# Kernel optimization log

Measured on AMD Instinct MI355X. Metric: run time of the kernel, lower is better.

The kernel has to match this reference:

```python
import jax, jax.numpy as jnp
import numpy as np

N = 100000
E = 3200000
IN_C, HID_C, LAT_C = 256, 256, 64
NEG_SLOPE = 0.01  # torch nn.LeakyReLU default


def gcn_conv(x, W, b, src, dst, norm):
    # x: [N, Fin], W: [Fin, Fout], src/dst: [E'] (self-loops included), norm: [E']
    h = x @ W                                   # [N, Fout]
    msg = h[src] * norm[:, None]                # gather + scale
    out = jax.ops.segment_sum(msg, dst, num_segments=N)  # scatter-add
    return out + b


def _with_self_loops(edge_index):
    loop = jnp.arange(N, dtype=edge_index.dtype)
    src = jnp.concatenate([edge_index[0], loop])
    dst = jnp.concatenate([edge_index[1], loop])
    return src, dst


def _sym_norm(src, dst):
    ones = jnp.ones(src.shape[0], dtype=jnp.float32)
    deg = jax.ops.segment_sum(ones, dst, num_segments=N)  # in-degree incl. self-loop
    dis = jnp.where(deg > 0, jax.lax.rsqrt(deg), 0.0)
    return dis[src] * dis[dst]


def setup_inputs() -> dict:
    key = jax.random.key(0)
    ks = jax.random.split(key, 8)
    x = jax.random.normal(ks[0], (N, IN_C), dtype=jnp.float32)
    edge_index = jax.random.randint(ks[1], (2, E), 0, N, dtype=jnp.int64)
    s = 1.0 / np.sqrt(IN_C)
    W_shared = jax.random.uniform(ks[2], (IN_C, HID_C), jnp.float32, -s, s)
    b_shared = jnp.zeros((HID_C,), jnp.float32)
    s2 = 1.0 / np.sqrt(HID_C)
    W_mu = jax.random.uniform(ks[3], (HID_C, LAT_C), jnp.float32, -s2, s2)
    b_mu = jnp.zeros((LAT_C,), jnp.float32)
    W_lv = jax.random.uniform(ks[4], (HID_C, LAT_C), jnp.float32, -s2, s2)
    b_lv = jnp.zeros((LAT_C,), jnp.float32)
    return {"x": x, "edge_index": edge_index,
            "W_shared": W_shared, "b_shared": b_shared,
            "W_mu": W_mu, "b_mu": b_mu,
            "W_lv": W_lv, "b_lv": b_lv}


def reference(x, W_shared, b_shared, W_mu, b_mu, W_lv, b_lv, edge_index):
    src, dst = _with_self_loops(edge_index)
    norm = _sym_norm(src, dst)
    h = gcn_conv(x, W_shared, b_shared, src, dst, norm)
    h = jnp.where(h >= 0, h, NEG_SLOPE * h)     # LeakyReLU(0.01)
    mu = gcn_conv(h, W_mu, b_mu, src, dst, norm)
    logvar = jnp.minimum(gcn_conv(h, W_lv, b_lv, src, dst, norm), 10.0)
    return (mu, logvar)
```

## Files before the change

kernel.cpp:

```cpp
#include <hip/hip_runtime.h>
#include <hip/hip_bf16.h>

#define N_NODES 100000
#define FEAT 256
#define NEG_SLOPE 0.01f
#define NBUK 782
#define BCAP 5120

using bf16x8 = __attribute__((ext_vector_type(8))) __bf16;
using f32x4  = __attribute__((ext_vector_type(4))) float;
using ushort8 = __attribute__((ext_vector_type(8))) unsigned short;

__device__ __forceinline__ unsigned short f2bf(float f) {
    unsigned int u = __float_as_uint(f);
    unsigned int r = u + 0x7fffu + ((u >> 16) & 1u);
    return (unsigned short)(r >> 16);
}
__device__ __forceinline__ void gload_lds16(const void* g, void* l) {
    __builtin_amdgcn_global_load_lds(
        (const __attribute__((address_space(1))) void*)g,
        (__attribute__((address_space(3))) void*)l, 16, 0, 0);
}
__device__ __forceinline__ void accum_row(float* acc, uint4 u, float qv) {
    unsigned int dw[4] = {u.x, u.y, u.z, u.w};
#pragma unroll
    for (int d = 0; d < 4; ++d) {
        acc[d * 4 + 0] += qv * (float)(dw[d] & 0xffu);
        acc[d * 4 + 1] += qv * (float)((dw[d] >> 8) & 0xffu);
        acc[d * 4 + 2] += qv * (float)((dw[d] >> 16) & 0xffu);
        acc[d * 4 + 3] += qv * (float)(dw[d] >> 24);
    }
}

__global__ void k_detect(const int* __restrict__ ei, int* __restrict__ flag) {
    if (threadIdx.x == 0) {
        int nz = 0;
        for (int i = 0; i < 64; ++i) nz |= ei[2 * i + 1];
        *flag = (nz == 0) ? 2 : 1;
    }
}

__global__ void k_bucket(const int* __restrict__ ei, const int* __restrict__ flag,
                         int* __restrict__ bcnt, int2* __restrict__ ebuf, int E) {
    __shared__ int lcnt[NBUK];
    __shared__ int lbase[NBUK];
    const int t = threadIdx.x;
    const int s = *flag;
    for (int i = t; i < NBUK; i += 256) lcnt[i] = 0;
    __syncthreads();
    const int per = (E + gridDim.x - 1) / gridDim.x;
    const int e0 = blockIdx.x * per;
    const int e1 = min(e0 + per, E);
    for (int e = e0 + t; e < e1; e += 256) {
        const int d = ei[(size_t)(E + e) * s];
        atomicAdd(&lcnt[d >> 7], 1);
    }
    __syncthreads();
    for (int i = t; i < NBUK; i += 256) {
        const int c = lcnt[i];
        lbase[i] = c ? atomicAdd(&bcnt[i], c) : 0;
        lcnt[i] = 0;
    }
    __syncthreads();
    for (int e = e0 + t; e < e1; e += 256) {
        const int sv = ei[(size_t)e * s];
        const int dv = ei[(size_t)(E + e) * s];
        const int b = dv >> 7;
        const int p = lbase[b] + atomicAdd(&lcnt[b], 1);
        if (p < BCAP) ebuf[(size_t)b * BCAP + p] = make_int2(sv, dv);
    }
}

__global__ void k_csr(const int2* __restrict__ ebuf, const int* __restrict__ bcnt,
                      int* __restrict__ csr, int* __restrict__ rowp0,
                      int* __restrict__ rowe, float* __restrict__ dis) {
    __shared__ int ncnt[128];
    __shared__ int nexcl[128];
    __shared__ int nstart[128];
    const int t = threadIdx.x;
    const int b = blockIdx.x;
    const int nb = b << 7;
    if (t < 128) ncnt[t] = 0;
    __syncthreads();
    const int cnt = min(bcnt[b], BCAP);
    const int2* eb = ebuf + (size_t)b * BCAP;
    for (int i = t; i < cnt; i += 256) atomicAdd(&ncnt[eb[i].y - nb], 1);
    __syncthreads();
    const int own = (t < 128) ? ncnt[t] : 0;
    const int region = (t < 128) ? ((own + 4) & ~3) : 0;
    if (t < 128) nexcl[t] = region;
    __syncthreads();
    for (int off = 1; off < 128; off <<= 1) {
        int v = 0;
        if (t < 128 && t >= off) v = nexcl[t - off];
        __syncthreads();
        if (t < 128) nexcl[t] += v;
        __syncthreads();
    }
    if (t < 128) {
        const int excl = nexcl[t] - region;
        const int v = nb + t;
        if (v < N_NODES) {
            rowp0[v] = b * BCAP + excl;
            rowe[v]  = b * BCAP + excl + region;
            dis[v]   = rsqrtf((float)(own + 1));
            if (excl < BCAP) csr[(size_t)b * BCAP + excl] = v;
            for (int i = own + 1; i < region; ++i)
                if (excl + i < BCAP) csr[(size_t)b * BCAP + excl + i] = N_NODES;
        }
        nstart[t] = excl + 1;
        ncnt[t] = 0;
    }
    __syncthreads();
    for (int i = t; i < cnt; i += 256) {
        const int2 e = eb[i];
        const int li = e.y - nb;
        const int p = nstart[li] + atomicAdd(&ncnt[li], 1);
        if (p < BCAP) csr[(size_t)b * BCAP + p] = e.x;
    }
}

__global__ void k_cvt_w(const float* __restrict__ Wsh, const float* __restrict__ Wmu,
                        const float* __restrict__ Wlv,
                        unsigned short* __restrict__ Wt, unsigned short* __restrict__ Wct) {
    const int i = blockIdx.x * 256 + threadIdx.x;
    {
        const int n = i >> 8, k = i & 255;
        Wt[(size_t)n * 256 + k] = f2bf(Wsh[(size_t)k * 256 + n]);
    }
    if (i < 128 * 256) {
        const int n = i >> 8, k = i & 255;
        const float v = (n < 64) ? Wmu[(size_t)k * 64 + n] : Wlv[(size_t)k * 64 + (n - 64)];
        Wct[(size_t)n * 256 + k] = f2bf(v);
    }
}

__global__ void __launch_bounds__(512) k_gemm256f(
        const float* __restrict__ A, const unsigned short* __restrict__ Bt,
        unsigned char* __restrict__ q8, float* __restrict__ qs,
        const float* __restrict__ scale, int M) {
    __shared__ __align__(16) unsigned short lA[128 * 32];
    __shared__ __align__(16) unsigned short lB[256 * 32];
    __shared__ float rmax[128][4];
    const int t = threadIdx.x;
    const int w = t >> 6, l = t & 63;
    const int wr = w >> 2, wc = w & 3;
    const int l15 = l & 15, lh = l >> 4;
    const int rowbase = blockIdx.x * 128;

    f32x4 acc[4][4];
#pragma unroll
    for (int mi = 0; mi < 4; ++mi)
#pragma unroll
        for (int nj = 0; nj < 4; ++nj)
            acc[mi][nj] = (f32x4){0.f, 0.f, 0.f, 0.f};

    const int ar = t >> 2, sl = t & 3;
    int grA = rowbase + ar; if (grA > M - 1) grA = M - 1;
    const float* aptr = A + (size_t)grA * FEAT + sl * 8;

#pragma unroll 1
    for (int ks = 0; ks < 8; ++ks) {
        const int k0 = ks * 32;
        gload_lds16(Bt + ((size_t)ar * FEAT + k0 + sl * 8), &lB[(size_t)t * 8]);
        gload_lds16(Bt + ((size_t)(128 + ar) * FEAT + k0 + sl * 8), &lB[(size_t)(512 + t) * 8]);
        float4 f0 = *reinterpret_cast<const float4*>(aptr + k0);
        float4 f1 = *reinterpret_cast<const float4*>(aptr + k0 + 4);
        ushort8 ua;
        ua[0] = f2bf(f0.x); ua[1] = f2bf(f0.y); ua[2] = f2bf(f0.z); ua[3] = f2bf(f0.w);
        ua[4] = f2bf(f1.x); ua[5] = f2bf(f1.y); ua[6] = f2bf(f1.z); ua[7] = f2bf(f1.w);
        *reinterpret_cast<ushort8*>(&lA[(size_t)ar * 32 + sl * 8]) = ua;
        asm volatile("s_waitcnt vmcnt(0)" ::: "memory");
        __syncthreads();

        bf16x8 a[4];
#pragma unroll
        for (int mi = 0; mi < 4; ++mi)
            a[mi] = *reinterpret_cast<const bf16x8*>(&lA[(wr * 64 + mi * 16 + l15) * 32 + lh * 8]);
#pragma unroll
        for (int nj = 0; nj < 4; ++nj) {
            bf16x8 b = *reinterpret_cast<const bf16x8*>(&lB[(wc * 64 + nj * 16 + l15) * 32 + lh * 8]);
#pragma unroll
            for (int mi = 0; mi < 4; ++mi)
                acc[mi][nj] = __builtin_amdgcn_mfma_f32_16x16x32_bf16(a[mi], b, acc[mi][nj], 0, 0, 0);
        }
        __syncthreads();
    }

#pragma unroll
    for (int mi = 0; mi < 4; ++mi) {
#pragma unroll
        for (int r = 0; r < 4; ++r) {
            const int rl = wr * 64 + mi * 16 + lh * 4 + r;
            int row = rowbase + rl; if (row > M - 1) row = M - 1;
            const float sc = scale[row];
            float m = 0.f;
#pragma unroll
            for (int nj = 0; nj < 4; ++nj) {
                acc[mi][nj][r] *= sc;
                m = fmaxf(m, fabsf(acc[mi][nj][r]));
            }
            m = fmaxf(m, __shfl_xor(m, 1, 64));
            m = fmaxf(m, __shfl_xor(m, 2, 64));
            m = fmaxf(m, __shfl_xor(m, 4, 64));
            m = fmaxf(m, __shfl_xor(m, 8, 64));
            if (l15 == 0) rmax[rl][wc] = m;
        }
    }
    __syncthreads();
#pragma unroll
    for (int mi = 0; mi < 4; ++mi) {
#pragma unroll
        for (int r = 0; r < 4; ++r) {
            const int rl = wr * 64 + mi * 16 + lh * 4 + r;
            const int row = rowbase + rl;
            const float fm = fmaxf(fmaxf(rmax[rl][0], rmax[rl][1]),
                                   fmaxf(rmax[rl][2], rmax[rl][3]));
            const float inv = (fm > 0.f) ? (127.0f / fm) : 0.f;
            if (row < M) {
                if (wc == 0 && l15 == 0) qs[row] = fm * (1.0f / 127.0f);
#pragma unroll
                for (int nj = 0; nj < 4; ++nj) {
                    int qv = (int)rintf(acc[mi][nj][r] * inv) + 128;
                    qv = min(max(qv, 0), 255);
                    q8[(size_t)row * 256 + wc * 64 + nj * 16 + l15] = (unsigned char)qv;
                }
            }
        }
    }
}

__global__ void k_gemm128q(const unsigned short* __restrict__ A,
                           const unsigned short* __restrict__ Bt,
                           unsigned char* __restrict__ q8, float* __restrict__ qs,
                           const float* __restrict__ scale, int M) {
    __shared__ __align__(16) unsigned short lA[64 * 32];
    __shared__ __align__(16) unsigned short lB[128 * 32];
    __shared__ float rmax[64][4];
    const int t = threadIdx.x;
    const int w = t >> 6, l = t & 63;
    const int l15 = l & 15, lh = l >> 4;
    const int rowbase = blockIdx.x * 64;

    f32x4 acc[4][2];
#pragma unroll
    for (int mi = 0; mi < 4; ++mi)
#pragma unroll
        for (int nj = 0; nj < 2; ++nj)
            acc[mi][nj] = (f32x4){0.f, 0.f, 0.f, 0.f};

    const int sr = t >> 2, sl = t & 3;
    int grA = rowbase + sr; if (grA > M - 1) grA = M - 1;

#pragma unroll 1
    for (int ks = 0; ks < 8; ++ks) {
        const int k0 = ks * 32;
        gload_lds16(A + ((size_t)grA * FEAT + k0 + sl * 8), &lA[(size_t)t * 8]);
#pragma unroll
        for (int j = 0; j < 2; ++j)
            gload_lds16(Bt + ((size_t)(j * 64 + sr) * FEAT + k0 + sl * 8),
                        &lB[(size_t)j * 2048 + (size_t)t * 8]);
        asm volatile("s_waitcnt vmcnt(0)" ::: "memory");
        __syncthreads();

        bf16x8 a[4];
#pragma unroll
        for (int mi = 0; mi < 4; ++mi)
            a[mi] = *reinterpret_cast<const bf16x8*>(&lA[(mi * 16 + l15) * 32 + lh * 8]);
#pragma unroll
        for (int nj = 0; nj < 2; ++nj) {
            bf16x8 b = *reinterpret_cast<const bf16x8*>(&lB[(w * 32 + nj * 16 + l15) * 32 + lh * 8]);
#pragma unroll
            for (int mi = 0; mi < 4; ++mi)
                acc[mi][nj] = __builtin_amdgcn_mfma_f32_16x16x32_bf16(a[mi], b, acc[mi][nj], 0, 0, 0);
        }
        __syncthreads();
    }

#pragma unroll
    for (int mi = 0; mi < 4; ++mi) {
#pragma unroll
        for (int r = 0; r < 4; ++r) {
            const int rl = mi * 16 + lh * 4 + r;
            int row = rowbase + rl; if (row > M - 1) row = M - 1;
            const float sc = scale[row];
            float m = 0.f;
#pragma unroll
            for (int nj = 0; nj < 2; ++nj) {
                acc[mi][nj][r] *= sc;
                m = fmaxf(m, fabsf(acc[mi][nj][r]));
            }
            m = fmaxf(m, __shfl_xor(m, 1, 64));
            m = fmaxf(m, __shfl_xor(m, 2, 64));
            m = fmaxf(m, __shfl_xor(m, 4, 64));
            m = fmaxf(m, __shfl_xor(m, 8, 64));
            if (l15 == 0) rmax[rl][w] = m;
        }
    }
    __syncthreads();
#pragma unroll
    for (int mi = 0; mi < 4; ++mi) {
#pragma unroll
        for (int r = 0; r < 4; ++r) {
            const int rl = mi * 16 + lh * 4 + r;
            const int row = rowbase + rl;
            const float fm = fmaxf(fmaxf(rmax[rl][0], rmax[rl][1]),
                                   fmaxf(rmax[rl][2], rmax[rl][3]));
            const float inv = (fm > 0.f) ? (127.0f / fm) : 0.f;
            if (row < M) {
                if (w == 0 && l15 == 0) qs[row] = fm * (1.0f / 127.0f);
#pragma unroll
                for (int nj = 0; nj < 2; ++nj) {
                    int qv = (int)rintf(acc[mi][nj][r] * inv) + 128;
                    qv = min(max(qv, 0), 255);
                    q8[(size_t)row * 128 + w * 32 + nj * 16 + l15] = (unsigned char)qv;
                }
            }
        }
    }
}

__global__ void k_agg1(const unsigned char* __restrict__ q8, const float* __restrict__ qs,
                       const int* __restrict__ rowp0, const int* __restrict__ rowe,
                       const int* __restrict__ csr,
                       const float* __restrict__ dis, const float* __restrict__ bias,
                       unsigned short* __restrict__ hout) {
    const int w = threadIdx.x >> 6, l = threadIdx.x & 63;
    const int v = blockIdx.x * 4 + w;
    if (v >= N_NODES) return;
    const int q = l >> 4, li = l & 15;
    const int p0 = rowp0[v], p1 = rowe[v];

    float acc[16];
#pragma unroll
    for (int j = 0; j < 16; ++j) acc[j] = 0.f;
    float sqs = 0.f;

    for (int g = p0 + q * 4; g < p1; g += 16) {
        const int4 s4 = *reinterpret_cast<const int4*>(&csr[g]);
        const float q0 = qs[s4.x], q1 = qs[s4.y], q2 = qs[s4.z], q3 = qs[s4.w];
        uint4 u0 = *reinterpret_cast<const uint4*>(&q8[(size_t)s4.x * 256 + li * 16]);
        uint4 u1 = *reinterpret_cast<const uint4*>(&q8[(size_t)s4.y * 256 + li * 16]);
        uint4 u2 = *reinterpret_cast<const uint4*>(&q8[(size_t)s4.z * 256 + li * 16]);
        uint4 u3 = *reinterpret_cast<const uint4*>(&q8[(size_t)s4.w * 256 + li * 16]);
        sqs += q0 + q1 + q2 + q3;
        accum_row(acc, u0, q0);
        accum_row(acc, u1, q1);
        accum_row(acc, u2, q2);
        accum_row(acc, u3, q3);
    }
#pragma unroll
    for (int j = 0; j < 16; ++j) acc[j] -= 128.f * sqs;

#pragma unroll
    for (int j = 0; j < 16; ++j) acc[j] += __shfl_xor(acc[j], 16, 64);
#pragma unroll
    for (int j = 0; j < 16; ++j) acc[j] += __shfl_xor(acc[j], 32, 64);

    if (l < 16) {
        const float dv = dis[v];
        const int c = l * 16;
        ushort8 r0, r1;
#pragma unroll
        for (int j = 0; j < 8; ++j) {
            float o = dv * acc[j] + bias[c + j];
            o = (o >= 0.f) ? o : NEG_SLOPE * o;
            r0[j] = f2bf(o);
        }
#pragma unroll
        for (int j = 0; j < 8; ++j) {
            float o = dv * acc[8 + j] + bias[c + 8 + j];
            o = (o >= 0.f) ? o : NEG_SLOPE * o;
            r1[j] = f2bf(o);
        }
        *reinterpret_cast<ushort8*>(&hout[(size_t)v * FEAT + c])     = r0;
        *reinterpret_cast<ushort8*>(&hout[(size_t)v * FEAT + c + 8]) = r1;
    }
}

__global__ void k_agg2(const unsigned char* __restrict__ q8, const float* __restrict__ qs,
                       const int* __restrict__ rowp0, const int* __restrict__ rowe,
                       const int* __restrict__ csr,
                       const float* __restrict__ dis,
                       const float* __restrict__ bmu, const float* __restrict__ blv,
                       float* __restrict__ out) {
    const int w = threadIdx.x >> 6, l = threadIdx.x & 63;
    const int v = blockIdx.x * 4 + w;
    if (v >= N_NODES) return;
    const int e = l >> 3, li = l & 7;
    const int p0 = rowp0[v], p1 = rowe[v];

    float acc[16];
#pragma unroll
    for (int j = 0; j < 16; ++j) acc[j] = 0.f;
    float sqs = 0.f;

    for (int g = p0 + e * 4; g < p1; g += 32) {
        const int4 s4 = *reinterpret_cast<const int4*>(&csr[g]);
        const float q0 = qs[s4.x], q1 = qs[s4.y], q2 = qs[s4.z], q3 = qs[s4.w];
        uint4 u0 = *reinterpret_cast<const uint4*>(&q8[(size_t)s4.x * 128 + li * 16]);
        uint4 u1 = *reinterpret_cast<const uint4*>(&q8[(size_t)s4.y * 128 + li * 16]);
        uint4 u2 = *reinterpret_cast<const uint4*>(&q8[(size_t)s4.z * 128 + li * 16]);
        uint4 u3 = *reinterpret_cast<const uint4*>(&q8[(size_t)s4.w * 128 + li * 16]);
        sqs += q0 + q1 + q2 + q3;
        accum_row(acc, u0, q0);
        accum_row(acc, u1, q1);
        accum_row(acc, u2, q2);
        accum_row(acc, u3, q3);
    }
#pragma unroll
    for (int j = 0; j < 16; ++j) acc[j] -= 128.f * sqs;

#pragma unroll
    for (int j = 0; j < 16; ++j) acc[j] += __shfl_xor(acc[j], 8, 64);
#pragma unroll
    for (int j = 0; j < 16; ++j) acc[j] += __shfl_xor(acc[j], 16, 64);
#pragma unroll
    for (int j = 0; j < 16; ++j) acc[j] += __shfl_xor(acc[j], 32, 64);

    if (l < 8) {
        const float dv = dis[v];
        const int c = l * 16;
        float o[16];
        if (c < 64) {
#pragma unroll
            for (int j = 0; j < 16; ++j) o[j] = dv * acc[j] + bmu[c + j];
            float* dst = &out[(size_t)v * 64 + c];
#pragma unroll
            for (int k = 0; k < 4; ++k) {
                float4 f = {o[k * 4], o[k * 4 + 1], o[k * 4 + 2], o[k * 4 + 3]};
                *reinterpret_cast<float4*>(dst + k * 4) = f;
            }
        } else {
            const int cc = c - 64;
#pragma unroll
            for (int j = 0; j < 16; ++j) o[j] = fminf(dv * acc[j] + blv[cc + j], 10.0f);
            float* dst = &out[(size_t)N_NODES * 64 + (size_t)v * 64 + cc];
#pragma unroll
            for (int k = 0; k < 4; ++k) {
                float4 f = {o[k * 4], o[k * 4 + 1], o[k * 4 + 2], o[k * 4 + 3]};
                *reinterpret_cast<float4*>(dst + k * 4) = f;
            }
        }
    }
}

extern "C" void kernel_launch(void* const* d_in, const int* in_sizes, int n_in,
                              void* d_out, int out_size, void* d_ws, size_t ws_size,
                              hipStream_t stream) {
    const float* x   = (const float*)d_in[0];
    const int*   ei  = (const int*)d_in[1];
    const float* Wsh = (const float*)d_in[2];
    const float* bsh = (const float*)d_in[3];
    const float* Wmu = (const float*)d_in[4];
    const float* bmu = (const float*)d_in[5];
    const float* Wlv = (const float*)d_in[6];
    const float* blv = (const float*)d_in[7];
    const int E = in_sizes[1] / 2;

    char* base = (char*)d_ws;
    size_t off = 0;
    auto take = [&](size_t bytes) -> char* {
        char* r = base + off;
        off += (bytes + 511) & ~(size_t)511;
        return r;
    };
    int*   flag  = (int*)take(4);
    int*   bcnt  = (int*)take((size_t)NBUK * 4);
    int*   rowp0 = (int*)take((size_t)N_NODES * 4);
    int*   rowe  = (int*)take((size_t)N_NODES * 4);
    float* dis   = (float*)take((size_t)N_NODES * 4);
    int*   csr   = (int*)take((size_t)NBUK * BCAP * 4);
    unsigned short* bufA = (unsigned short*)take((size_t)N_NODES * FEAT * 2);
    unsigned short* Wt   = (unsigned short*)take(256 * 256 * 2);
    unsigned short* Wct  = (unsigned short*)take(128 * 256 * 2);
    unsigned char* q8A = (unsigned char*)take(((size_t)N_NODES + 1) * 256);
    float*         qsA = (float*)take(((size_t)N_NODES + 1) * 4);
    unsigned char* q8B = (unsigned char*)take(((size_t)N_NODES + 1) * 128);
    float*         qsB = (float*)take(((size_t)N_NODES + 1) * 4);
    int2* ebuf = (int2*)q8A;

    hipMemsetAsync(bcnt, 0, (size_t)NBUK * 4, stream);
    k_detect<<<1, 64, 0, stream>>>(ei, flag);
    k_bucket<<<256, 256, 0, stream>>>(ei, flag, bcnt, ebuf, E);
    k_csr<<<NBUK, 256, 0, stream>>>(ebuf, bcnt, csr, rowp0, rowe, dis);
    k_cvt_w<<<256, 256, 0, stream>>>(Wsh, Wmu, Wlv, Wt, Wct);
    hipMemsetAsync(qsA + N_NODES, 0, 4, stream);
    hipMemsetAsync(qsB + N_NODES, 0, 4, stream);
    k_gemm256f<<<(N_NODES + 127) / 128, 512, 0, stream>>>(x, Wt, q8A, qsA, dis, N_NODES);
    k_agg1<<<(N_NODES + 3) / 4, 256, 0, stream>>>(q8A, qsA, rowp0, rowe, csr, dis, bsh, bufA);
    k_gemm128q<<<(N_NODES + 63) / 64, 256, 0, stream>>>(bufA, Wct, q8B, qsB, dis, N_NODES);
    k_agg2<<<(N_NODES + 3) / 4, 256, 0, stream>>>(q8B, qsB, rowp0, rowe, csr, dis, bmu, blv, (float*)d_out);
}
```

Baseline: 444.3 us.

## Fuse edge bucketing with first GEMM and defer degree scaling to aggregation

Bucketing blocks and the first GEMM's blocks now run in a single launch, so the edge sort overlaps with the matmul. This is possible because the GEMM no longer needs the degree scale: per-row quantization runs on the unscaled output, and the dis factor is folded into a new per-node scale qd computed in k_csr. Setup work (flag detection, counter zeroing, weight conversion, sentinel zeroing) is merged into one init kernel, removing several launches and memsets. The byte-to-float conversion in accumulation now uses v_cvt_f32_ubyteN. The bucket edge buffer is moved from the q8A region to bufA, since q8A is now written concurrently with bucketing.

```diff
diff --git a/kernel.cpp b/kernel.cpp
--- a/kernel.cpp
+++ b/kernel.cpp
@@ -6,6 +6,8 @@
 #define NEG_SLOPE 0.01f
 #define NBUK 782
 #define BCAP 5120
+#define NBB 256
+#define NGB 782
 
 using bf16x8 = __attribute__((ext_vector_type(8))) __bf16;
 using f32x4  = __attribute__((ext_vector_type(4))) float;
@@ -25,55 +27,175 @@
     unsigned int dw[4] = {u.x, u.y, u.z, u.w};
 #pragma unroll
     for (int d = 0; d < 4; ++d) {
-        acc[d * 4 + 0] += qv * (float)(dw[d] & 0xffu);
-        acc[d * 4 + 1] += qv * (float)((dw[d] >> 8) & 0xffu);
-        acc[d * 4 + 2] += qv * (float)((dw[d] >> 16) & 0xffu);
-        acc[d * 4 + 3] += qv * (float)(dw[d] >> 24);
-    }
-}
-
-__global__ void k_detect(const int* __restrict__ ei, int* __restrict__ flag) {
-    if (threadIdx.x == 0) {
-        int nz = 0;
-        for (int i = 0; i < 64; ++i) nz |= ei[2 * i + 1];
-        *flag = (nz == 0) ? 2 : 1;
-    }
-}
-
-__global__ void k_bucket(const int* __restrict__ ei, const int* __restrict__ flag,
-                         int* __restrict__ bcnt, int2* __restrict__ ebuf, int E) {
+        float f0, f1, f2, f3;
+        asm("v_cvt_f32_ubyte0 %0, %1" : "=v"(f0) : "v"(dw[d]));
+        asm("v_cvt_f32_ubyte1 %0, %1" : "=v"(f1) : "v"(dw[d]));
+        asm("v_cvt_f32_ubyte2 %0, %1" : "=v"(f2) : "v"(dw[d]));
+        asm("v_cvt_f32_ubyte3 %0, %1" : "=v"(f3) : "v"(dw[d]));
+        acc[d * 4 + 0] += qv * f0;
+        acc[d * 4 + 1] += qv * f1;
+        acc[d * 4 + 2] += qv * f2;
+        acc[d * 4 + 3] += qv * f3;
+    }
+}
+
+__global__ void k_init(const int* __restrict__ ei, int* __restrict__ flag,
+                       int* __restrict__ bcnt, float* __restrict__ qd,
+                       float* __restrict__ qsB,
+                       const float* __restrict__ Wsh, const float* __restrict__ Wmu,
+                       const float* __restrict__ Wlv,
+                       unsigned short* __restrict__ Wt, unsigned short* __restrict__ Wct) {
+    const int b = blockIdx.x, t = threadIdx.x;
+    if (b == 0) {
+        if (t == 0) {
+            int nz = 0;
+            for (int i = 0; i < 64; ++i) nz |= ei[2 * i + 1];
+            *flag = (nz == 0) ? 2 : 1;
+            qd[N_NODES]  = 0.f;
+            qsB[N_NODES] = 0.f;
+        }
+        for (int i = t; i < NBUK; i += 256) bcnt[i] = 0;
+    } else {
+        const int i = (b - 1) * 256 + t;
+        {
+            const int n = i >> 8, k = i & 255;
+            Wt[(size_t)n * 256 + k] = f2bf(Wsh[(size_t)k * 256 + n]);
+        }
+        if (i < 128 * 256) {
+            const int n = i >> 8, k = i & 255;
+            const float v = (n < 64) ? Wmu[(size_t)k * 64 + n] : Wlv[(size_t)k * 64 + (n - 64)];
+            Wct[(size_t)n * 256 + k] = f2bf(v);
+        }
+    }
+}
+
+__global__ void __launch_bounds__(512) k_phaseA(
+        const int* __restrict__ ei, const int* __restrict__ flag,
+        int* __restrict__ bcnt, int2* __restrict__ ebuf, int E,
+        const float* __restrict__ A, const unsigned short* __restrict__ Bt,
+        unsigned char* __restrict__ q8, float* __restrict__ qs, int M) {
     __shared__ int lcnt[NBUK];
     __shared__ int lbase[NBUK];
+    __shared__ __align__(16) unsigned short lA[128 * 32];
+    __shared__ __align__(16) unsigned short lB[256 * 32];
+    __shared__ float rmax[128][4];
     const int t = threadIdx.x;
-    const int s = *flag;
-    for (int i = t; i < NBUK; i += 256) lcnt[i] = 0;
+
+    if (blockIdx.x < NBB) {
+        const int s = *flag;
+        for (int i = t; i < NBUK; i += 512) lcnt[i] = 0;
+        __syncthreads();
+        const int per = (E + NBB - 1) / NBB;
+        const int e0 = blockIdx.x * per;
+        const int e1 = min(e0 + per, E);
+        for (int e = e0 + t; e < e1; e += 512) {
+            const int d = ei[(size_t)(E + e) * s];
+            atomicAdd(&lcnt[d >> 7], 1);
+        }
+        __syncthreads();
+        for (int i = t; i < NBUK; i += 512) {
+            const int c = lcnt[i];
+            lbase[i] = c ? atomicAdd(&bcnt[i], c) : 0;
+            lcnt[i] = 0;
+        }
+        __syncthreads();
+        for (int e = e0 + t; e < e1; e += 512) {
+            const int sv = ei[(size_t)e * s];
+            const int dv = ei[(size_t)(E + e) * s];
+            const int b = dv >> 7;
+            const int p = lbase[b] + atomicAdd(&lcnt[b], 1);
+            if (p < BCAP) ebuf[(size_t)b * BCAP + p] = make_int2(sv, dv);
+        }
+        return;
+    }
+
+    const int bid = blockIdx.x - NBB;
+    const int w = t >> 6, l = t & 63;
+    const int wr = w >> 2, wc = w & 3;
+    const int l15 = l & 15, lh = l >> 4;
+    const int rowbase = bid * 128;
+
+    f32x4 acc[4][4];
+#pragma unroll
+    for (int mi = 0; mi < 4; ++mi)
+#pragma unroll
+        for (int nj = 0; nj < 4; ++nj)
+            acc[mi][nj] = (f32x4){0.f, 0.f, 0.f, 0.f};
+
+    const int ar = t >> 2, sl = t & 3;
+    int grA = rowbase + ar; if (grA > M - 1) grA = M - 1;
+    const float* aptr = A + (size_t)grA * FEAT + sl * 8;
+
+#pragma unroll 1
+    for (int ks = 0; ks < 8; ++ks) {
+        const int k0 = ks * 32;
+        gload_lds16(Bt + ((size_t)ar * FEAT + k0 + sl * 8), &lB[(size_t)t * 8]);
+        gload_lds16(Bt + ((size_t)(128 + ar) * FEAT + k0 + sl * 8), &lB[(size_t)(512 + t) * 8]);
+        float4 f0 = *reinterpret_cast<const float4*>(aptr + k0);
+        float4 f1 = *reinterpret_cast<const float4*>(aptr + k0 + 4);
+        ushort8 ua;
+        ua[0] = f2bf(f0.x); ua[1] = f2bf(f0.y); ua[2] = f2bf(f0.z); ua[3] = f2bf(f0.w);
+        ua[4] = f2bf(f1.x); ua[5] = f2bf(f1.y); ua[6] = f2bf(f1.z); ua[7] = f2bf(f1.w);
+        *reinterpret_cast<ushort8*>(&lA[(size_t)ar * 32 + sl * 8]) = ua;
+        asm volatile("s_waitcnt vmcnt(0)" ::: "memory");
+        __syncthreads();
+
+        bf16x8 a[4];
+#pragma unroll
+        for (int mi = 0; mi < 4; ++mi)
+            a[mi] = *reinterpret_cast<const bf16x8*>(&lA[(wr * 64 + mi * 16 + l15) * 32 + lh * 8]);
+#pragma unroll
+        for (int nj = 0; nj < 4; ++nj) {
+            bf16x8 b = *reinterpret_cast<const bf16x8*>(&lB[(wc * 64 + nj * 16 + l15) * 32 + lh * 8]);
+#pragma unroll
+            for (int mi = 0; mi < 4; ++mi)
+                acc[mi][nj] = __builtin_amdgcn_mfma_f32_16x16x32_bf16(a[mi], b, acc[mi][nj], 0, 0, 0);
+        }
+        __syncthreads();
+    }
+
+#pragma unroll
+    for (int mi = 0; mi < 4; ++mi) {
+#pragma unroll
+        for (int r = 0; r < 4; ++r) {
+            const int rl = wr * 64 + mi * 16 + lh * 4 + r;
+            float m = 0.f;
+#pragma unroll
+            for (int nj = 0; nj < 4; ++nj) m = fmaxf(m, fabsf(acc[mi][nj][r]));
+            m = fmaxf(m, __shfl_xor(m, 1, 64));
+            m = fmaxf(m, __shfl_xor(m, 2, 64));
+            m = fmaxf(m, __shfl_xor(m, 4, 64));
+            m = fmaxf(m, __shfl_xor(m, 8, 64));
+            if (l15 == 0) rmax[rl][wc] = m;
+        }
+    }
     __syncthreads();
-    const int per = (E + gridDim.x - 1) / gridDim.x;
-    const int e0 = blockIdx.x * per;
-    const int e1 = min(e0 + per, E);
-    for (int e = e0 + t; e < e1; e += 256) {
-        const int d = ei[(size_t)(E + e) * s];
-        atomicAdd(&lcnt[d >> 7], 1);
-    }
-    __syncthreads();
-    for (int i = t; i < NBUK; i += 256) {
-        const int c = lcnt[i];
-        lbase[i] = c ? atomicAdd(&bcnt[i], c) : 0;
-        lcnt[i] = 0;
-    }
-    __syncthreads();
-    for (int e = e0 + t; e < e1; e += 256) {
-        const int sv = ei[(size_t)e * s];
-        const int dv = ei[(size_t)(E + e) * s];
-        const int b = dv >> 7;
-        const int p = lbase[b] + atomicAdd(&lcnt[b], 1);
-        if (p < BCAP) ebuf[(size_t)b * BCAP + p] = make_int2(sv, dv);
+#pragma unroll
+    for (int mi = 0; mi < 4; ++mi) {
+#pragma unroll
+        for (int r = 0; r < 4; ++r) {
+            const int rl = wr * 64 + mi * 16 + lh * 4 + r;
+            const int row = rowbase + rl;
+            const float fm = fmaxf(fmaxf(rmax[rl][0], rmax[rl][1]),
+                                   fmaxf(rmax[rl][2], rmax[rl][3]));
+            const float inv = (fm > 0.f) ? (127.0f / fm) : 0.f;
+            if (row < M) {
+                if (wc == 0 && l15 == 0) qs[row] = fm * (1.0f / 127.0f);
+#pragma unroll
+                for (int nj = 0; nj < 4; ++nj) {
+                    int qv = (int)rintf(acc[mi][nj][r] * inv) + 128;
+                    qv = min(max(qv, 0), 255);
+                    q8[(size_t)row * 256 + wc * 64 + nj * 16 + l15] = (unsigned char)qv;
+                }
+            }
+        }
     }
 }
 
 __global__ void k_csr(const int2* __restrict__ ebuf, const int* __restrict__ bcnt,
                       int* __restrict__ csr, int* __restrict__ rowp0,
-                      int* __restrict__ rowe, float* __restrict__ dis) {
+                      int* __restrict__ rowe, float* __restrict__ dis,
+                      const float* __restrict__ qsA, float* __restrict__ qd) {
     __shared__ int ncnt[128];
     __shared__ int nexcl[128];
     __shared__ int nstart[128];
@@ -103,7 +225,9 @@
         if (v < N_NODES) {
             rowp0[v] = b * BCAP + excl;
             rowe[v]  = b * BCAP + excl + region;
-            dis[v]   = rsqrtf((float)(own + 1));
+            const float dv = rsqrtf((float)(own + 1));
+            dis[v] = dv;
+            qd[v]  = qsA[v] * dv;
             if (excl < BCAP) csr[(size_t)b * BCAP + excl] = v;
             for (int i = own + 1; i < region; ++i)
                 if (excl + i < BCAP) csr[(size_t)b * BCAP + excl + i] = N_NODES;
@@ -117,116 +241,6 @@
         const int li = e.y - nb;
         const int p = nstart[li] + atomicAdd(&ncnt[li], 1);
         if (p < BCAP) csr[(size_t)b * BCAP + p] = e.x;
-    }
-}
-
-__global__ void k_cvt_w(const float* __restrict__ Wsh, const float* __restrict__ Wmu,
-                        const float* __restrict__ Wlv,
-                        unsigned short* __restrict__ Wt, unsigned short* __restrict__ Wct) {
-    const int i = blockIdx.x * 256 + threadIdx.x;
-    {
-        const int n = i >> 8, k = i & 255;
-        Wt[(size_t)n * 256 + k] = f2bf(Wsh[(size_t)k * 256 + n]);
-    }
-    if (i < 128 * 256) {
-        const int n = i >> 8, k = i & 255;
-        const float v = (n < 64) ? Wmu[(size_t)k * 64 + n] : Wlv[(size_t)k * 64 + (n - 64)];
-        Wct[(size_t)n * 256 + k] = f2bf(v);
-    }
-}
-
-__global__ void __launch_bounds__(512) k_gemm256f(
-        const float* __restrict__ A, const unsigned short* __restrict__ Bt,
-        unsigned char* __restrict__ q8, float* __restrict__ qs,
-        const float* __restrict__ scale, int M) {
-    __shared__ __align__(16) unsigned short lA[128 * 32];
-    __shared__ __align__(16) unsigned short lB[256 * 32];
-    __shared__ float rmax[128][4];
-    const int t = threadIdx.x;
-    const int w = t >> 6, l = t & 63;
-    const int wr = w >> 2, wc = w & 3;
-    const int l15 = l & 15, lh = l >> 4;
-    const int rowbase = blockIdx.x * 128;
-
-    f32x4 acc[4][4];
-#pragma unroll
-    for (int mi = 0; mi < 4; ++mi)
-#pragma unroll
-        for (int nj = 0; nj < 4; ++nj)
-            acc[mi][nj] = (f32x4){0.f, 0.f, 0.f, 0.f};
-
-    const int ar = t >> 2, sl = t & 3;
-    int grA = rowbase + ar; if (grA > M - 1) grA = M - 1;
-    const float* aptr = A + (size_t)grA * FEAT + sl * 8;
-
-#pragma unroll 1
-    for (int ks = 0; ks < 8; ++ks) {
-        const int k0 = ks * 32;
-        gload_lds16(Bt + ((size_t)ar * FEAT + k0 + sl * 8), &lB[(size_t)t * 8]);
-        gload_lds16(Bt + ((size_t)(128 + ar) * FEAT + k0 + sl * 8), &lB[(size_t)(512 + t) * 8]);
-        float4 f0 = *reinterpret_cast<const float4*>(aptr + k0);
-        float4 f1 = *reinterpret_cast<const float4*>(aptr + k0 + 4);
-        ushort8 ua;
-        ua[0] = f2bf(f0.x); ua[1] = f2bf(f0.y); ua[2] = f2bf(f0.z); ua[3] = f2bf(f0.w);
-        ua[4] = f2bf(f1.x); ua[5] = f2bf(f1.y); ua[6] = f2bf(f1.z); ua[7] = f2bf(f1.w);
-        *reinterpret_cast<ushort8*>(&lA[(size_t)ar * 32 + sl * 8]) = ua;
-        asm volatile("s_waitcnt vmcnt(0)" ::: "memory");
-        __syncthreads();
-
-        bf16x8 a[4];
-#pragma unroll
-        for (int mi = 0; mi < 4; ++mi)
-            a[mi] = *reinterpret_cast<const bf16x8*>(&lA[(wr * 64 + mi * 16 + l15) * 32 + lh * 8]);
-#pragma unroll
-        for (int nj = 0; nj < 4; ++nj) {
-            bf16x8 b = *reinterpret_cast<const bf16x8*>(&lB[(wc * 64 + nj * 16 + l15) * 32 + lh * 8]);
-#pragma unroll
-            for (int mi = 0; mi < 4; ++mi)
-                acc[mi][nj] = __builtin_amdgcn_mfma_f32_16x16x32_bf16(a[mi], b, acc[mi][nj], 0, 0, 0);
-        }
-        __syncthreads();
-    }
-
-#pragma unroll
-    for (int mi = 0; mi < 4; ++mi) {
-#pragma unroll
-        for (int r = 0; r < 4; ++r) {
-            const int rl = wr * 64 + mi * 16 + lh * 4 + r;
-            int row = rowbase + rl; if (row > M - 1) row = M - 1;
-            const float sc = scale[row];
-            float m = 0.f;
-#pragma unroll
-            for (int nj = 0; nj < 4; ++nj) {
-                acc[mi][nj][r] *= sc;
-                m = fmaxf(m, fabsf(acc[mi][nj][r]));
-            }
-            m = fmaxf(m, __shfl_xor(m, 1, 64));
-            m = fmaxf(m, __shfl_xor(m, 2, 64));
-            m = fmaxf(m, __shfl_xor(m, 4, 64));
-            m = fmaxf(m, __shfl_xor(m, 8, 64));
-            if (l15 == 0) rmax[rl][wc] = m;
-        }
-    }
-    __syncthreads();
-#pragma unroll
-    for (int mi = 0; mi < 4; ++mi) {
-#pragma unroll
-        for (int r = 0; r < 4; ++r) {
-            const int rl = wr * 64 + mi * 16 + lh * 4 + r;
-            const int row = rowbase + rl;
-            const float fm = fmaxf(fmaxf(rmax[rl][0], rmax[rl][1]),
-                                   fmaxf(rmax[rl][2], rmax[rl][3]));
-            const float inv = (fm > 0.f) ? (127.0f / fm) : 0.f;
-            if (row < M) {
-                if (wc == 0 && l15 == 0) qs[row] = fm * (1.0f / 127.0f);
-#pragma unroll
-                for (int nj = 0; nj < 4; ++nj) {
-                    int qv = (int)rintf(acc[mi][nj][r] * inv) + 128;
-                    qv = min(max(qv, 0), 255);
-                    q8[(size_t)row * 256 + wc * 64 + nj * 16 + l15] = (unsigned char)qv;
-                }
-            }
-        }
     }
 }
 
@@ -320,7 +334,7 @@
     }
 }
 
-__global__ void k_agg1(const unsigned char* __restrict__ q8, const float* __restrict__ qs,
+__global__ void k_agg1(const unsigned char* __restrict__ q8, const float* __restrict__ qd,
                        const int* __restrict__ rowp0, const int* __restrict__ rowe,
                        const int* __restrict__ csr,
                        const float* __restrict__ dis, const float* __restrict__ bias,
@@ -338,7 +352,7 @@
 
     for (int g = p0 + q * 4; g < p1; g += 16) {
         const int4 s4 = *reinterpret_cast<const int4*>(&csr[g]);
-        const float q0 = qs[s4.x], q1 = qs[s4.y], q2 = qs[s4.z], q3 = qs[s4.w];
+        const float q0 = qd[s4.x], q1 = qd[s4.y], q2 = qd[s4.z], q3 = qd[s4.w];
         uint4 u0 = *reinterpret_cast<const uint4*>(&q8[(size_t)s4.x * 256 + li * 16]);
         uint4 u1 = *reinterpret_cast<const uint4*>(&q8[(size_t)s4.y * 256 + li * 16]);
         uint4 u2 = *reinterpret_cast<const uint4*>(&q8[(size_t)s4.z * 256 + li * 16]);
@@ -470,6 +484,7 @@
     int*   rowp0 = (int*)take((size_t)N_NODES * 4);
     int*   rowe  = (int*)take((size_t)N_NODES * 4);
     float* dis   = (float*)take((size_t)N_NODES * 4);
+    float* qd    = (float*)take(((size_t)N_NODES + 1) * 4);
     int*   csr   = (int*)take((size_t)NBUK * BCAP * 4);
     unsigned short* bufA = (unsigned short*)take((size_t)N_NODES * FEAT * 2);
     unsigned short* Wt   = (unsigned short*)take(256 * 256 * 2);
@@ -478,17 +493,12 @@
     float*         qsA = (float*)take(((size_t)N_NODES + 1) * 4);
     unsigned char* q8B = (unsigned char*)take(((size_t)N_NODES + 1) * 128);
     float*         qsB = (float*)take(((size_t)N_NODES + 1) * 4);
-    int2* ebuf = (int2*)q8A;
-
-    hipMemsetAsync(bcnt, 0, (size_t)NBUK * 4, stream);
-    k_detect<<<1, 64, 0, stream>>>(ei, flag);
-    k_bucket<<<256, 256, 0, stream>>>(ei, flag, bcnt, ebuf, E);
-    k_csr<<<NBUK, 256, 0, stream>>>(ebuf, bcnt, csr, rowp0, rowe, dis);
-    k_cvt_w<<<256, 256, 0, stream>>>(Wsh, Wmu, Wlv, Wt, Wct);
-    hipMemsetAsync(qsA + N_NODES, 0, 4, stream);
-    hipMemsetAsync(qsB + N_NODES, 0, 4, stream);
-    k_gemm256f<<<(N_NODES + 127) / 128, 512, 0, stream>>>(x, Wt, q8A, qsA, dis, N_NODES);
-    k_agg1<<<(N_NODES + 3) / 4, 256, 0, stream>>>(q8A, qsA, rowp0, rowe, csr, dis, bsh, bufA);
+    int2* ebuf = (int2*)bufA;
+
+    k_init<<<257, 256, 0, stream>>>(ei, flag, bcnt, qd, qsB, Wsh, Wmu, Wlv, Wt, Wct);
+    k_phaseA<<<NBB + NGB, 512, 0, stream>>>(ei, flag, bcnt, ebuf, E, x, Wt, q8A, qsA, N_NODES);
+    k_csr<<<NBUK, 256, 0, stream>>>(ebuf, bcnt, csr, rowp0, rowe, dis, qsA, qd);
+    k_agg1<<<(N_NODES + 3) / 4, 256, 0, stream>>>(q8A, qd, rowp0, rowe, csr, dis, bsh, bufA);
     k_gemm128q<<<(N_NODES + 63) / 64, 256, 0, stream>>>(bufA, Wct, q8B, qsB, dis, N_NODES);
     k_agg2<<<(N_NODES + 3) / 4, 256, 0, stream>>>(q8B, qsB, rowp0, rowe, csr, dis, bmu, blv, (float*)d_out);
 }
```

New measurement: 379.7 us. 1.17x faster.
